# Optimization experiments

Hardware: AMD Instinct MI355X
Metric: run time of the kernel (lower is better)

Reference implementation:

```python
import jax, jax.numpy as jnp
import numpy as np

B, S, D = 4, 2048, 1024
H, ADIM = 16, 64
HID = H * ADIM  # 1024


def setup_inputs() -> dict:
    key = jax.random.key(0)
    k1, k2, k3, k4 = jax.random.split(key, 4)
    iQ = jax.random.normal(k1, (B, S, D), dtype=jnp.float32)
    mask = jax.random.randint(k2, (B, S, S), 0, 2).astype(bool)
    Wa = jax.random.normal(k3, (3 * HID, D), dtype=jnp.float32) * (1.0 / np.sqrt(D))
    Wo = jax.random.normal(k4, (HID, HID), dtype=jnp.float32) * (1.0 / np.sqrt(HID))
    return {"iQ": iQ, "mask": mask, "Wa": Wa, "Wo": Wo}


def reference(iQ, mask, Wa, Wo):
    b, s, _ = iQ.shape
    # fused QKV projection: [B,S,3*HID]
    qkv = jnp.einsum("bsd,ed->bse", iQ, Wa)
    q, k, v = jnp.split(qkv, 3, axis=-1)
    # [B,S,HID] -> [B,H,S,ADIM]
    to_heads = lambda t: t.reshape(b, s, H, ADIM).transpose(0, 2, 1, 3)
    q, k, v = to_heads(q), to_heads(k), to_heads(v)
    scores = jnp.einsum("bhqd,bhkd->bhqk", q, k) / np.sqrt(ADIM).astype(np.float32)
    scores = jnp.where(mask[:, None, :, :], jnp.float32(-1e32), scores)
    attn = jax.nn.softmax(scores, axis=-1)
    o = jnp.einsum("bhqk,bhkd->bhqd", attn, v)
    o = o.transpose(0, 2, 1, 3).reshape(b, s, HID)
    return jnp.einsum("bse,oe->bso", o, Wo)
```

## Files before the change

### kernel.cpp

```cpp
#include <hip/hip_runtime.h>
#include <hip/hip_bf16.h>

typedef __bf16 bf16;
typedef __bf16 bfrag __attribute__((ext_vector_type(8)));
typedef __bf16 bf16x4 __attribute__((ext_vector_type(4)));
typedef float f32x4 __attribute__((ext_vector_type(4)));

constexpr int Bc = 4, Sc = 2048, Hc = 16, ADc = 64, HIDc = 1024;
constexpr size_t QKV_ELEMS = (size_t)Bc * Hc * Sc * ADc;

__device__ __forceinline__ void gload_lds16(const void* g, void* lds) {
  __builtin_amdgcn_global_load_lds(
      (const __attribute__((address_space(1))) unsigned int*)g,
      (__attribute__((address_space(3))) unsigned int*)lds, 16, 0, 0);
}

__device__ __forceinline__ bfrag ldb(const bf16* p) {
  return *(const bfrag*)p;
}

__global__ __launch_bounds__(256) void f2b(const float* __restrict__ s,
                                           bf16* __restrict__ d) {
  const size_t i = ((size_t)blockIdx.x * 256 + threadIdx.x) * 8;
  const float4 a = *(const float4*)(s + i);
  const float4 b = *(const float4*)(s + i + 4);
  bfrag o = {(bf16)a.x, (bf16)a.y, (bf16)a.z, (bf16)a.w,
             (bf16)b.x, (bf16)b.y, (bf16)b.z, (bf16)b.w};
  *(bfrag*)(d + i) = o;
}

template <int MODE>
__global__ __launch_bounds__(256) void gemm_bt(
    const bf16* __restrict__ A,
    const bf16* __restrict__ Bm,
    bf16* __restrict__ C0,
    bf16* __restrict__ C1,
    bf16* __restrict__ C2,
    float* __restrict__ Cf,
    int Kdim, int Ndim)
{
  __shared__ __align__(16) bf16 As[128 * 32];
  __shared__ __align__(16) bf16 Bs[128 * 32];

  const int tid  = threadIdx.x;
  const int wave = tid >> 6;
  const int lane = tid & 63;
  const int n16  = lane & 15;
  const int quad = lane >> 4;
  const int wm   = wave & 1;
  const int wn   = wave >> 1;
  const int m0   = blockIdx.y * 128;
  const int n0   = blockIdx.x * 128;

  const f32x4 fzero = {0.f, 0.f, 0.f, 0.f};
  f32x4 acc[4][4];
#pragma unroll
  for (int i = 0; i < 4; ++i)
#pragma unroll
    for (int j = 0; j < 4; ++j) acc[i][j] = fzero;

  const int lcol = (lane & 3) * 8;

  for (int k0 = 0; k0 < Kdim; k0 += 32) {
#pragma unroll
    for (int c = 0; c < 2; ++c) {
      const int chunk = wave * 2 + c;
      const int row   = chunk * 16 + (lane >> 2);
      const bf16* agp;
      if (MODE == 0) {
        agp = A + (size_t)(m0 + row) * Kdim + k0 + lcol;
      } else {
        const int gs = m0 + row;
        const int h  = k0 >> 6;
        agp = A + (((size_t)(gs >> 11) * Hc + h) * Sc + (gs & 2047)) * ADc
                + (k0 & 63) + lcol;
      }
      gload_lds16(agp, (char*)As + chunk * 1024);
      gload_lds16(Bm + (size_t)(n0 + row) * Kdim + k0 + lcol,
                  (char*)Bs + chunk * 1024);
    }
    __syncthreads();

    bfrag af[4], bf[4];
#pragma unroll
    for (int i = 0; i < 4; ++i)
      af[i] = ldb(As + (wm * 64 + i * 16 + n16) * 32 + quad * 8);
#pragma unroll
    for (int j = 0; j < 4; ++j)
      bf[j] = ldb(Bs + (wn * 64 + j * 16 + n16) * 32 + quad * 8);
#pragma unroll
    for (int i = 0; i < 4; ++i)
#pragma unroll
      for (int j = 0; j < 4; ++j)
        acc[i][j] = __builtin_amdgcn_mfma_f32_16x16x32_bf16(af[i], bf[j], acc[i][j], 0, 0, 0);
    __syncthreads();
  }

#pragma unroll
  for (int i = 0; i < 4; ++i) {
    const int grow = m0 + wm * 64 + i * 16 + quad * 4;
#pragma unroll
    for (int j = 0; j < 4; ++j) {
      const int col_local = wn * 64 + j * 16 + n16;
#pragma unroll
      for (int r = 0; r < 4; ++r) {
        const int row = grow + r;
        const float v = acc[i][j][r];
        if (MODE == 1) {
          Cf[(size_t)row * Ndim + n0 + col_local] = v;
        } else {
          const int seg = n0 >> 10;
          const int hid = (n0 & 1023) + col_local;
          const int h = hid >> 6, a = hid & 63;
          const int bi = row >> 11, s = row & 2047;
          if (seg == 0)
            C0[(((size_t)bi * Hc + h) * Sc + s) * ADc + a] = (bf16)(v * 0.125f);
          else if (seg == 1)
            C1[(((size_t)bi * Hc + h) * Sc + s) * ADc + a] = (bf16)v;
          else
            C2[(((size_t)bi * Hc + h) * ADc + a) * Sc + s] = (bf16)v;
        }
      }
    }
  }
}

__global__ __launch_bounds__(256) void mask_pack(const int* __restrict__ mask,
                                                 unsigned* __restrict__ bits) {
  const int w = blockIdx.x * 256 + threadIdx.x;
  const int4* p = (const int4*)(mask + (size_t)w * 32);
  unsigned out = 0;
#pragma unroll
  for (int i = 0; i < 8; ++i) {
    int4 m = p[i];
    out |= (unsigned)(m.x != 0) << (i * 4);
    out |= (unsigned)(m.y != 0) << (i * 4 + 1);
    out |= (unsigned)(m.z != 0) << (i * 4 + 2);
    out |= (unsigned)(m.w != 0) << (i * 4 + 3);
  }
  bits[w] = out;
}

__global__ __launch_bounds__(512) void attn(
    const bf16* __restrict__ Qw,
    const bf16* __restrict__ Kw,
    const bf16* __restrict__ Vtw,
    const unsigned* __restrict__ mbits,
    bf16* __restrict__ Ow)
{
  __shared__ __align__(16) bf16 Ks[64 * 64];
  __shared__ __align__(16) bf16 Vs[64 * 64];
  __shared__ __align__(16) bf16 Plds[8][16][72];

  const int tid  = threadIdx.x;
  const int wave = tid >> 6, lane = tid & 63;
  const int n16  = lane & 15, quad = lane >> 4;
  const int q4   = quad * 4;
  const int bh   = blockIdx.x >> 4, qb = blockIdx.x & 15;
  const int b    = bh >> 4;
  const int q0   = qb * 128 + wave * 16;

  const int srow = tid >> 3;
  const int scol = (tid & 7) * 8;
  const bf16* gK = Kw  + ((size_t)bh * Sc + srow) * ADc + scol;
  const bf16* gV = Vtw + ((size_t)bh * ADc + srow) * Sc + scol;
  bf16* lK = Ks + srow * 64 + (scol ^ ((srow & 7) * 8));
  bf16* lV = Vs + srow * 64 + (scol ^ ((srow & 7) * 8));

  const int fsw  = (n16 & 7) * 8;
  const int off0 = (quad * 8) ^ fsw;
  const int off1 = (32 + quad * 8) ^ fsw;

  const bf16* qrow = Qw + ((size_t)bh * Sc + q0 + n16) * ADc;
  const bfrag qf0 = ldb(qrow + quad * 8);
  const bfrag qf1 = ldb(qrow + 32 + quad * 8);

  const f32x4 fzero = {0.f, 0.f, 0.f, 0.f};
  float li = 0.f;
  f32x4 of[4];
#pragma unroll
  for (int nt = 0; nt < 4; ++nt) of[nt] = fzero;

  const unsigned* mq = mbits + ((size_t)b * Sc + q0 + n16) * (Sc / 32);

  {
    bfrag k0r = ldb(gK);
    bfrag v0r = ldb(gV);
    *(bfrag*)lK = k0r;
    *(bfrag*)lV = v0r;
  }
  __syncthreads();

  for (int kt = 0; kt < Sc / 64; ++kt) {
    const int kn0 = ((kt + 1) & 31) * 64;
    const bfrag kpre = ldb(gK + (size_t)kn0 * ADc);
    const bfrag vpre = ldb(gV + kn0);

    const uint2 mwv = *(const uint2*)(mq + kt * 2);

    f32x4 sf[4];
#pragma unroll
    for (int nt = 0; nt < 4; ++nt) {
      const bf16* kr = Ks + (nt * 16 + n16) * 64;
      const bfrag kf0 = ldb(kr + off0);
      const bfrag kf1 = ldb(kr + off1);
      f32x4 c = fzero;
      c = __builtin_amdgcn_mfma_f32_16x16x32_bf16(kf0, qf0, c, 0, 0, 0);
      c = __builtin_amdgcn_mfma_f32_16x16x32_bf16(kf1, qf1, c, 0, 0, 0);
      sf[nt] = c;
    }

    bf16* pl = &Plds[wave][0][0];
    __asm__ volatile("" ::: "memory");
#pragma unroll
    for (int nt = 0; nt < 4; ++nt) {
      const unsigned word = (nt & 2) ? mwv.y : mwv.x;
      bf16x4 t;
#pragma unroll
      for (int r = 0; r < 4; ++r) {
        float p = __expf(sf[nt][r]);
        if ((word >> ((nt & 1) * 16 + q4 + r)) & 1u) p = 0.f;
        li += p;
        t[r] = (bf16)p;
      }
      *(bf16x4*)(pl + n16 * 72 + nt * 16 + q4) = t;
    }
    __asm__ volatile("" ::: "memory");
    const bfrag pf0 = ldb(pl + n16 * 72 + quad * 8);
    const bfrag pf1 = ldb(pl + n16 * 72 + 32 + quad * 8);

#pragma unroll
    for (int nt = 0; nt < 4; ++nt) {
      const bf16* vr = Vs + (nt * 16 + n16) * 64;
      const bfrag vf0 = ldb(vr + off0);
      const bfrag vf1 = ldb(vr + off1);
      of[nt] = __builtin_amdgcn_mfma_f32_16x16x32_bf16(pf0, vf0, of[nt], 0, 0, 0);
      of[nt] = __builtin_amdgcn_mfma_f32_16x16x32_bf16(pf1, vf1, of[nt], 0, 0, 0);
    }

    __syncthreads();
    *(bfrag*)lK = kpre;
    *(bfrag*)lV = vpre;
    __syncthreads();
  }

  float s = li;
  s += __shfl_xor(s, 16);
  s += __shfl_xor(s, 32);
  const float inv = 1.f / s;
#pragma unroll
  for (int r = 0; r < 4; ++r) {
    const float invr = __shfl(inv, q4 + r, 64);
    const int q = q0 + q4 + r;
    bf16* orow = Ow + ((size_t)bh * Sc + q) * ADc;
#pragma unroll
    for (int nt = 0; nt < 4; ++nt)
      orow[nt * 16 + n16] = (bf16)(of[nt][r] * invr);
  }
}

extern "C" void kernel_launch(void* const* d_in, const int* in_sizes, int n_in,
                              void* d_out, int out_size, void* d_ws, size_t ws_size,
                              hipStream_t stream) {
  const float* iQ = (const float*)d_in[0];
  const int* mask = (const int*)d_in[1];
  const float* Wa = (const float*)d_in[2];
  const float* Wo = (const float*)d_in[3];
  float* out      = (float*)d_out;

  bf16* iQb       = (bf16*)d_out;
  bf16* Wab       = iQb + QKV_ELEMS;
  unsigned* mbits = (unsigned*)(Wab + 3145728);
  bf16* Qw  = (bf16*)d_ws;
  bf16* Kw  = Qw + QKV_ELEMS;
  bf16* Vtw = Kw + QKV_ELEMS;
  bf16* Wob = Vtw + QKV_ELEMS;

  f2b<<<dim3(8388608 / 2048), 256, 0, stream>>>(iQ, iQb);
  f2b<<<dim3(3145728 / 2048), 256, 0, stream>>>(Wa, Wab);
  f2b<<<dim3(1048576 / 2048), 256, 0, stream>>>(Wo, Wob);
  mask_pack<<<dim3((Bc * Sc * Sc / 32) / 256), 256, 0, stream>>>(mask, mbits);
  gemm_bt<0><<<dim3(24, 64), 256, 0, stream>>>(iQb, Wab, Qw, Kw, Vtw, nullptr, 1024, 3072);
  attn<<<dim3(Bc * Hc * 16), 512, 0, stream>>>(Qw, Kw, Vtw, mbits, Qw);
  gemm_bt<1><<<dim3(8, 64), 256, 0, stream>>>(Qw, Wob, nullptr, nullptr, nullptr, out, 1024, 1024);
}
```

Measured before the change: 376.0 us.

## Use 32x32x16 MFMA in attention with register-resident P via permlane32 swap

```diff
diff --git a/kernel.cpp b/kernel.cpp
--- a/kernel.cpp
+++ b/kernel.cpp
@@ -3,8 +3,10 @@
 
 typedef __bf16 bf16;
 typedef __bf16 bfrag __attribute__((ext_vector_type(8)));
-typedef __bf16 bf16x4 __attribute__((ext_vector_type(4)));
+typedef __bf16 bf16x2 __attribute__((ext_vector_type(2)));
 typedef float f32x4 __attribute__((ext_vector_type(4)));
+typedef float f32x16 __attribute__((ext_vector_type(16)));
+typedef unsigned u32x2 __attribute__((ext_vector_type(2)));
 
 constexpr int Bc = 4, Sc = 2048, Hc = 16, ADc = 64, HIDc = 1024;
 constexpr size_t QKV_ELEMS = (size_t)Bc * Hc * Sc * ADc;
@@ -17,6 +19,25 @@
 
 __device__ __forceinline__ bfrag ldb(const bf16* p) {
   return *(const bfrag*)p;
+}
+
+__device__ __forceinline__ unsigned pack2(float lo, float hi) {
+  union { bf16x2 h; unsigned u; } c;
+  c.h = bf16x2{(bf16)lo, (bf16)hi};
+  return c.u;
+}
+
+__device__ __forceinline__ void plswap(unsigned& a, unsigned& b) {
+  u32x2 r = __builtin_amdgcn_permlane32_swap(a, b, false, false);
+  a = r.x;
+  b = r.y;
+}
+
+__device__ __forceinline__ f32x16 zero16() {
+  f32x16 z;
+#pragma unroll
+  for (int i = 0; i < 16; ++i) z[i] = 0.f;
+  return z;
 }
 
 __global__ __launch_bounds__(256) void f2b(const float* __restrict__ s,
@@ -141,7 +162,7 @@
   bits[w] = out;
 }
 
-__global__ __launch_bounds__(512) void attn(
+__global__ __launch_bounds__(512, 4) void attn(
     const bf16* __restrict__ Qw,
     const bf16* __restrict__ Kw,
     const bf16* __restrict__ Vtw,
@@ -150,15 +171,14 @@
 {
   __shared__ __align__(16) bf16 Ks[64 * 64];
   __shared__ __align__(16) bf16 Vs[64 * 64];
-  __shared__ __align__(16) bf16 Plds[8][16][72];
 
   const int tid  = threadIdx.x;
   const int wave = tid >> 6, lane = tid & 63;
-  const int n16  = lane & 15, quad = lane >> 4;
-  const int q4   = quad * 4;
-  const int bh   = blockIdx.x >> 4, qb = blockIdx.x & 15;
+  const int l31  = lane & 31, hi = lane >> 5;
+  const int sw   = lane & 7;
+  const int bh   = blockIdx.x >> 3, qb = blockIdx.x & 7;
   const int b    = bh >> 4;
-  const int q0   = qb * 128 + wave * 16;
+  const int q0w  = qb * 256 + wave * 32;
 
   const int srow = tid >> 3;
   const int scol = (tid & 7) * 8;
@@ -167,25 +187,20 @@
   bf16* lK = Ks + srow * 64 + (scol ^ ((srow & 7) * 8));
   bf16* lV = Vs + srow * 64 + (scol ^ ((srow & 7) * 8));
 
-  const int fsw  = (n16 & 7) * 8;
-  const int off0 = (quad * 8) ^ fsw;
-  const int off1 = (32 + quad * 8) ^ fsw;
-
-  const bf16* qrow = Qw + ((size_t)bh * Sc + q0 + n16) * ADc;
-  const bfrag qf0 = ldb(qrow + quad * 8);
-  const bfrag qf1 = ldb(qrow + 32 + quad * 8);
-
-  const f32x4 fzero = {0.f, 0.f, 0.f, 0.f};
+  const bf16* qrow = Qw + ((size_t)bh * Sc + q0w + l31) * ADc + hi * 8;
+  bfrag qf[4];
+#pragma unroll
+  for (int ks = 0; ks < 4; ++ks) qf[ks] = ldb(qrow + ks * 16);
+
+  f32x16 of0 = zero16();
+  f32x16 of1 = zero16();
   float li = 0.f;
-  f32x4 of[4];
-#pragma unroll
-  for (int nt = 0; nt < 4; ++nt) of[nt] = fzero;
-
-  const unsigned* mq = mbits + ((size_t)b * Sc + q0 + n16) * (Sc / 32);
+
+  const unsigned* mq = mbits + ((size_t)b * Sc + q0w + l31) * (Sc / 32);
 
   {
-    bfrag k0r = ldb(gK);
-    bfrag v0r = ldb(gV);
+    const bfrag k0r = ldb(gK);
+    const bfrag v0r = ldb(gV);
     *(bfrag*)lK = k0r;
     *(bfrag*)lV = v0r;
   }
@@ -198,44 +213,42 @@
 
     const uint2 mwv = *(const uint2*)(mq + kt * 2);
 
-    f32x4 sf[4];
-#pragma unroll
-    for (int nt = 0; nt < 4; ++nt) {
-      const bf16* kr = Ks + (nt * 16 + n16) * 64;
-      const bfrag kf0 = ldb(kr + off0);
-      const bfrag kf1 = ldb(kr + off1);
-      f32x4 c = fzero;
-      c = __builtin_amdgcn_mfma_f32_16x16x32_bf16(kf0, qf0, c, 0, 0, 0);
-      c = __builtin_amdgcn_mfma_f32_16x16x32_bf16(kf1, qf1, c, 0, 0, 0);
-      sf[nt] = c;
-    }
-
-    bf16* pl = &Plds[wave][0][0];
-    __asm__ volatile("" ::: "memory");
-#pragma unroll
-    for (int nt = 0; nt < 4; ++nt) {
-      const unsigned word = (nt & 2) ? mwv.y : mwv.x;
-      bf16x4 t;
-#pragma unroll
-      for (int r = 0; r < 4; ++r) {
-        float p = __expf(sf[nt][r]);
-        if ((word >> ((nt & 1) * 16 + q4 + r)) & 1u) p = 0.f;
-        li += p;
-        t[r] = (bf16)p;
-      }
-      *(bf16x4*)(pl + n16 * 72 + nt * 16 + q4) = t;
-    }
-    __asm__ volatile("" ::: "memory");
-    const bfrag pf0 = ldb(pl + n16 * 72 + quad * 8);
-    const bfrag pf1 = ldb(pl + n16 * 72 + 32 + quad * 8);
-
-#pragma unroll
-    for (int nt = 0; nt < 4; ++nt) {
-      const bf16* vr = Vs + (nt * 16 + n16) * 64;
-      const bfrag vf0 = ldb(vr + off0);
-      const bfrag vf1 = ldb(vr + off1);
-      of[nt] = __builtin_amdgcn_mfma_f32_16x16x32_bf16(pf0, vf0, of[nt], 0, 0, 0);
-      of[nt] = __builtin_amdgcn_mfma_f32_16x16x32_bf16(pf1, vf1, of[nt], 0, 0, 0);
+#pragma unroll
+    for (int nt = 0; nt < 2; ++nt) {
+      f32x16 sf = zero16();
+#pragma unroll
+      for (int ks = 0; ks < 4; ++ks) {
+        const bfrag kf = ldb(Ks + (nt * 32 + l31) * 64 + (((2 * ks + hi) ^ sw) * 8));
+        sf = __builtin_amdgcn_mfma_f32_32x32x16_bf16(kf, qf[ks], sf, 0, 0, 0);
+      }
+
+      const unsigned w = (nt ? mwv.y : mwv.x) >> (hi * 4);
+      unsigned D[8];
+#pragma unroll
+      for (int m = 0; m < 8; ++m) {
+        const int r0 = 2 * m, r1 = r0 + 1;
+        float p0 = __expf(sf[r0]);
+        float p1 = __expf(sf[r1]);
+        if ((w >> ((r0 & 3) + 8 * (r0 >> 2))) & 1u) p0 = 0.f;
+        if ((w >> ((r1 & 3) + 8 * (r1 >> 2))) & 1u) p1 = 0.f;
+        li += p0 + p1;
+        D[m] = pack2(p0, p1);
+      }
+
+#pragma unroll
+      for (int a = 0; a < 2; ++a) {
+        unsigned w0 = D[4 * a + 0], w2 = D[4 * a + 2];
+        plswap(w0, w2);
+        unsigned w1 = D[4 * a + 1], w3 = D[4 * a + 3];
+        plswap(w1, w3);
+        union { unsigned u[4]; bfrag f; } pu;
+        pu.u[0] = w0; pu.u[1] = w1; pu.u[2] = w2; pu.u[3] = w3;
+        const int vg = ((4 * nt + 2 * a + hi) ^ sw) * 8;
+        const bfrag vf0 = ldb(Vs + l31 * 64 + vg);
+        of0 = __builtin_amdgcn_mfma_f32_32x32x16_bf16(pu.f, vf0, of0, 0, 0, 0);
+        const bfrag vf1 = ldb(Vs + (32 + l31) * 64 + vg);
+        of1 = __builtin_amdgcn_mfma_f32_32x32x16_bf16(pu.f, vf1, of1, 0, 0, 0);
+      }
     }
 
     __syncthreads();
@@ -244,18 +257,15 @@
     __syncthreads();
   }
 
-  float s = li;
-  s += __shfl_xor(s, 16);
-  s += __shfl_xor(s, 32);
+  const float s = li + __shfl_xor(li, 32);
   const float inv = 1.f / s;
 #pragma unroll
-  for (int r = 0; r < 4; ++r) {
-    const float invr = __shfl(inv, q4 + r, 64);
-    const int q = q0 + q4 + r;
-    bf16* orow = Ow + ((size_t)bh * Sc + q) * ADc;
-#pragma unroll
-    for (int nt = 0; nt < 4; ++nt)
-      orow[nt * 16 + n16] = (bf16)(of[nt][r] * invr);
+  for (int r = 0; r < 16; ++r) {
+    const int query = (r & 3) + 8 * (r >> 2) + 4 * hi;
+    const float invr = __shfl(inv, query);
+    bf16* orow = Ow + ((size_t)bh * Sc + q0w + query) * ADc + l31;
+    orow[0]  = (bf16)(of0[r] * invr);
+    orow[32] = (bf16)(of1[r] * invr);
   }
 }
 
@@ -281,6 +291,6 @@
   f2b<<<dim3(1048576 / 2048), 256, 0, stream>>>(Wo, Wob);
   mask_pack<<<dim3((Bc * Sc * Sc / 32) / 256), 256, 0, stream>>>(mask, mbits);
   gemm_bt<0><<<dim3(24, 64), 256, 0, stream>>>(iQb, Wab, Qw, Kw, Vtw, nullptr, 1024, 3072);
-  attn<<<dim3(Bc * Hc * 16), 512, 0, stream>>>(Qw, Kw, Vtw, mbits, Qw);
+  attn<<<dim3(Bc * Hc * 8), 512, 0, stream>>>(Qw, Kw, Vtw, mbits, Qw);
   gemm_bt<1><<<dim3(8, 64), 256, 0, stream>>>(Qw, Wob, nullptr, nullptr, nullptr, out, 1024, 1024);
 }
```

Result: no change. 374.3 us (-0.5%).
